# Performance work log

Measured on AMD Instinct MI355X. Metric: run time of the kernel, lower is better.

## Reference

```python
import jax, jax.numpy as jnp
import numpy as np

CUTOFF = 3.5          # angular_cutoff (init kwarg)
EPS = 1e-7            # keras.backend.epsilon()
CLIP_MIN = 1e-10      # tf.clip_by_value min on Carnot denominators
B, N = 8, 32
MLP_DIMS = [(9, 64), (64, 64), (64, 64), (64, 64), (64, 64), (64, 128), (128, 256)]


def _he(key, fan_in, fan_out):
    return jax.random.normal(key, (fan_in, fan_out), jnp.float32) * np.float32(np.sqrt(2.0 / fan_in))


def setup_inputs() -> dict:
    key = jax.random.key(0)
    k_pos, k_sp, k_w, k_b = jax.random.split(key, 4)
    # realistic symmetric distance matrix with zero diagonal, from random 3D positions
    pos = jax.random.uniform(k_pos, (B, N, 3), jnp.float32) * 9.0
    diff = pos[:, :, None, :] - pos[:, None, :, :]
    D = jnp.sqrt(jnp.sum(diff * diff, axis=-1) + 1e-12)
    D = D * (1.0 - jnp.eye(N, dtype=jnp.float32))
    species = jax.random.randint(k_sp, (B, N), 1, 10).astype(jnp.float32)
    inp = {"distance_matrices": D, "num_species_batch": species}
    for i, (fi, fo) in enumerate(MLP_DIMS):
        inp[f"W{i}"] = _he(jax.random.fold_in(k_w, i), fi, fo)
        inp[f"b{i}"] = jax.random.normal(jax.random.fold_in(k_b, i), (fo,), jnp.float32) * 0.01
    return inp


def _ang_mlp(x, W0, b0, W1, b1, W2, b2, W3, b3, W4, b4, W5, b5, W6, b6):
    # residual MLP: 9 -> 64 (x5, two residual adds) -> 128 -> 256, all tanh
    x_res = jnp.tanh(x @ W0 + b0)
    x1 = jnp.tanh(x_res @ W1 + b1)
    xb1 = x1 + x_res
    x2 = jnp.tanh(xb1 @ W2 + b2)
    x3 = jnp.tanh(x2 @ W3 + b3)
    x4 = jnp.tanh(x3 @ W4 + b4)
    xb2 = x4 + xb1
    xb3 = jnp.tanh(xb2 @ W5 + b5)
    return jnp.tanh(xb3 @ W6 + b6)


def _forward(D, S, W0, b0, W1, b1, W2, b2, W3, b3, W4, b4, W5, b5, W6, b6):
    n = D.shape[-1]
    ji, ki = jnp.triu_indices(n, k=1)                       # P = n(n-1)/2 ordered pairs j<k
    cm = (D < CUTOFF) & (D != 0.0)                          # [B,N,N]
    mask = cm[:, :, ji] & cm[:, :, ki]                      # [B,N,P] valid triplets (i;j,k)
    R_ij = D[:, :, ji]                                      # [B,N,P]
    R_ik = D[:, :, ki]
    R_jk = jnp.broadcast_to(D[:, ji, ki][:, None, :], R_ij.shape)
    z_i = jnp.broadcast_to(S[:, :, None], R_ij.shape)
    z_j = jnp.broadcast_to(S[:, ji][:, None, :], R_ij.shape)
    z_k = jnp.broadcast_to(S[:, ki][:, None, :], R_ij.shape)
    # Carnot formula for the three cosines of the triangle (i,j,k)
    clip = lambda d: jnp.maximum(d, CLIP_MIN)
    c_i = (R_ij**2 + R_ik**2 - R_jk**2) / clip(2.0 * R_ij * R_ik)
    c_j = (R_ij**2 + R_jk**2 - R_ik**2) / clip(2.0 * R_ij * R_jk)
    c_k = (R_ik**2 + R_jk**2 - R_ij**2) / clip(2.0 * R_ik * R_jk)
    geo = jnp.stack([
        R_ij + R_ik + R_jk,
        R_ij * R_ik + R_ij * R_jk + R_ik * R_jk,
        R_ij * R_ik * R_jk,
    ], axis=-1)                                             # [B,N,P,3]
    chem = jnp.stack([
        z_i + z_j + z_k,
        c_i + c_j + c_k,
        z_i * (z_j + z_k) + z_j * z_k - c_i * (c_j + c_k) - c_j * c_k,
        z_i * (c_j + c_k) + c_i * (z_j + z_k) + z_j * c_k + c_j * z_k,
        z_i * (z_j * z_k - c_j * c_k) - c_i * (z_j * c_k + c_j * z_k),
        z_i * (z_j * c_k + c_j * z_k) + c_i * (z_j * z_k - c_j * c_k),
    ], axis=-1)                                             # [B,N,P,6]
    geo = geo / (jnp.linalg.norm(geo, axis=-1, keepdims=True) + EPS)
    chem = chem / (jnp.linalg.norm(chem, axis=-1, keepdims=True) + EPS)
    feat = jnp.concatenate([geo, chem], axis=-1)            # [B,N,P,9]
    out = _ang_mlp(feat, W0, b0, W1, b1, W2, b2, W3, b3, W4, b4, W5, b5, W6, b6)  # [B,N,P,256]
    f_c = lambda d: 0.5 * jnp.cos(np.float32(np.pi) * d / CUTOFF) + 0.5
    w = jnp.where(mask, f_c(R_ij) * f_c(R_ik), 0.0)[..., None]
    GA = jnp.sum(out * w, axis=2)                           # scatter-add over triplets -> [B,N,256]
    return GA / (jnp.linalg.norm(GA, axis=-1, keepdims=True) + EPS)


def reference(distance_matrices, num_species_batch, W0, b0, W1, b1, W2, b2, W3, b3, W4, b4, W5, b5, W6, b6):
    return _forward(distance_matrices, num_species_batch, W0, b0, W1, b1, W2, b2, W3, b3, W4, b4, W5, b5, W6, b6)
```

## Files before the change

### kernel.cpp

```cpp
#include <hip/hip_runtime.h>
#include <math.h>

#define NB 8
#define NA 32
#define NCELL 256
#define NPAIR 496
#define SLOT 496
#define FST 10
#define TC 16
#define XS 20
#define NQ 8
#define CUTOFF_F 3.5f
#define EPS_F 1e-7f
#define CLIP_MIN_F 1e-10f
#define PI_F 3.14159274101257324f

#define PIPE_BAR4() do { \
    asm volatile("s_waitcnt lgkmcnt(0) vmcnt(4)" ::: "memory"); \
    __builtin_amdgcn_s_barrier(); \
    __builtin_amdgcn_sched_barrier(0); \
} while (0)
#define PIPE_BAR0() do { \
    asm volatile("s_waitcnt lgkmcnt(0) vmcnt(0)" ::: "memory"); \
    __builtin_amdgcn_s_barrier(); \
    __builtin_amdgcn_sched_barrier(0); \
} while (0)

__device__ __forceinline__ float fast_tanh(float x) {
    const float ax = fabsf(x);
    const float t = exp2f(fminf(2.8853900817779268f * ax, 30.0f));
    const float r = (t - 1.0f) * __builtin_amdgcn_rcpf(t + 1.0f);
    return __int_as_float((__float_as_int(x) & 0x80000000) | __float_as_int(r));
}

__global__ __launch_bounds__(256) void aev_feat(
    const float* __restrict__ D, const float* __restrict__ S,
    float* __restrict__ feat, int* __restrict__ count, float* __restrict__ GA)
{
    __shared__ float Dm[NA][NA];
    __shared__ float Sv[NA];
    __shared__ int s_T;
    const int tid = threadIdx.x;
    const int cell = blockIdx.x;
    const int b = cell >> 5, i = cell & 31;

    for (int idx = tid; idx < NA * NA; idx += 256)
        ((float*)Dm)[idx] = D[b * NA * NA + idx];
    if (tid < NA) Sv[tid] = S[b * NA + tid];
    if (tid == 0) s_T = 0;
    GA[cell * 256 + tid] = 0.f;
    __syncthreads();

    for (int p = tid; p < NPAIR; p += 256) {
        int rem = p, j = 0;
        while (rem >= 31 - j) { rem -= 31 - j; ++j; }
        const int k = j + 1 + rem;
        const float dij = Dm[i][j], dik = Dm[i][k];
        if (dij < CUTOFF_F && dij != 0.f && dik < CUTOFF_F && dik != 0.f) {
            const int slot = atomicAdd(&s_T, 1);
            const float Rij = dij, Rik = dik, Rjk = Dm[j][k];
            const float zi = Sv[i], zj = Sv[j], zk = Sv[k];
            const float ci = (Rij*Rij + Rik*Rik - Rjk*Rjk) / fmaxf(2.f*Rij*Rik, CLIP_MIN_F);
            const float cj = (Rij*Rij + Rjk*Rjk - Rik*Rik) / fmaxf(2.f*Rij*Rjk, CLIP_MIN_F);
            const float ck = (Rik*Rik + Rjk*Rjk - Rij*Rij) / fmaxf(2.f*Rik*Rjk, CLIP_MIN_F);
            float g0 = Rij + Rik + Rjk;
            float g1 = Rij*Rik + Rij*Rjk + Rik*Rjk;
            float g2 = Rij*Rik*Rjk;
            const float gn = sqrtf(g0*g0 + g1*g1 + g2*g2) + EPS_F;
            float h0 = zi + zj + zk;
            float h1 = ci + cj + ck;
            float h2 = zi*(zj + zk) + zj*zk - ci*(cj + ck) - cj*ck;
            float h3 = zi*(cj + ck) + ci*(zj + zk) + zj*ck + cj*zk;
            float h4 = zi*(zj*zk - cj*ck) - ci*(zj*ck + cj*zk);
            float h5 = zi*(zj*ck + cj*zk) + ci*(zj*zk - cj*ck);
            const float hn = sqrtf(h0*h0 + h1*h1 + h2*h2 + h3*h3 + h4*h4 + h5*h5) + EPS_F;
            const float fcij = 0.5f * cosf(PI_F * Rij / CUTOFF_F) + 0.5f;
            const float fcik = 0.5f * cosf(PI_F * Rik / CUTOFF_F) + 0.5f;
            float* fp = &feat[(cell * SLOT + slot) * FST];
            fp[0] = g0 / gn; fp[1] = g1 / gn; fp[2] = g2 / gn;
            fp[3] = h0 / hn; fp[4] = h1 / hn; fp[5] = h2 / hn;
            fp[6] = h3 / hn; fp[7] = h4 / hn; fp[8] = h5 / hn;
            fp[9] = fcij * fcik;
        }
    }
    __syncthreads();
    if (tid == 0) count[cell] = s_T;
}

__device__ __forceinline__ void cp_async16(const float* g, float* l) {
    __builtin_amdgcn_global_load_lds(
        (const __attribute__((address_space(1))) unsigned int*)g,
        (__attribute__((address_space(3))) unsigned int*)l, 16, 0, 0);
}

__device__ __forceinline__ void stage16k(const float* __restrict__ g,
                                         float* __restrict__ buf, int tid) {
    const int lane = tid & 63, w = tid >> 6;
#pragma unroll
    for (int r = 0; r < 4; ++r) {
        const int off = (w * 4 + r) * 256;
        cp_async16(g + off + lane * 4, buf + off);
    }
}

template<int K, bool RES>
__device__ __forceinline__ void compute64(
    const float* __restrict__ Wl, float bb,
    const float* __restrict__ X, float* __restrict__ Y,
    const float* __restrict__ R, int tid)
{
    const int fi = tid & 63;
    const int xo = (tid >> 6) * 4;
    float a0 = bb, a1 = bb, a2 = bb, a3 = bb;
#pragma unroll 4
    for (int k = 0; k < K; ++k) {
        const float4 xv = *(const float4*)&X[k * XS + xo];
        const float w = Wl[k * 64 + fi];
        a0 += xv.x * w; a1 += xv.y * w; a2 += xv.z * w; a3 += xv.w * w;
    }
    float4 y;
    y.x = fast_tanh(a0); y.y = fast_tanh(a1); y.z = fast_tanh(a2); y.w = fast_tanh(a3);
    if (RES) {
        const float4 r = *(const float4*)&R[fi * XS + xo];
        y.x += r.x; y.y += r.y; y.z += r.z; y.w += r.w;
    }
    *(float4*)&Y[fi * XS + xo] = y;
}

__device__ __forceinline__ void compute5_part(
    const float* __restrict__ Wl , const float* __restrict__ X,
    int k0, float (&a)[4][2], int tid)
{
    const int f = (tid & 31) * 4;
    const int t = (tid >> 5) * 2;
#pragma unroll 4
    for (int k = 0; k < 32; ++k) {
        const float4 wv = *(const float4*)&Wl[k * 128 + f];
        const float2 xv = *(const float2*)&X[(k0 + k) * XS + t];
        a[0][0] += wv.x * xv.x; a[0][1] += wv.x * xv.y;
        a[1][0] += wv.y * xv.x; a[1][1] += wv.y * xv.y;
        a[2][0] += wv.z * xv.x; a[2][1] += wv.z * xv.y;
        a[3][0] += wv.w * xv.x; a[3][1] += wv.w * xv.y;
    }
}

__device__ __forceinline__ void compute6_part(
    const float* __restrict__ Wl , const float* __restrict__ X,
    float (&c)[4][4], int f, int t)
{
#pragma unroll 2
    for (int k = 0; k < 16; ++k) {
        const float4 wv = *(const float4*)&Wl[k * 256 + f];
        const float4 xv = *(const float4*)&X[k * XS + t];
        c[0][0] += wv.x * xv.x; c[0][1] += wv.x * xv.y; c[0][2] += wv.x * xv.z; c[0][3] += wv.x * xv.w;
        c[1][0] += wv.y * xv.x; c[1][1] += wv.y * xv.y; c[1][2] += wv.y * xv.z; c[1][3] += wv.y * xv.w;
        c[2][0] += wv.z * xv.x; c[2][1] += wv.z * xv.y; c[2][2] += wv.z * xv.z; c[2][3] += wv.z * xv.w;
        c[3][0] += wv.w * xv.x; c[3][1] += wv.w * xv.y; c[3][2] += wv.w * xv.z; c[3][3] += wv.w * xv.w;
    }
}

__global__ __launch_bounds__(256) void aev_mlp(
    const float* __restrict__ feat, const int* __restrict__ count,
    const float* __restrict__ W0, const float* __restrict__ b0,
    const float* __restrict__ W1, const float* __restrict__ b1,
    const float* __restrict__ W2, const float* __restrict__ b2,
    const float* __restrict__ W3, const float* __restrict__ b3,
    const float* __restrict__ W4, const float* __restrict__ b4,
    const float* __restrict__ W5, const float* __restrict__ b5,
    const float* __restrict__ W6, const float* __restrict__ b6,
    float* __restrict__ GA)
{
    __shared__ __align__(16) float WB0[4096];
    __shared__ __align__(16) float WB1[4096];
    __shared__ __align__(16) float WB2[4096];
    __shared__ __align__(16) float W0s[576];
    __shared__ __align__(16) float Xs[9 * XS];
    __shared__ __align__(16) float U0[64 * XS];
    __shared__ __align__(16) float U1[64 * XS];
    __shared__ __align__(16) float U2[64 * XS];
    __shared__ float wsh[TC];

    const int tid = threadIdx.x;
    const int cell = blockIdx.x & 255;
    const int q = blockIdx.x >> 8;
    const int T = count[cell];
    const int nch = (T + TC - 1) / TC;
    if (q >= nch) return;

    const int fi64 = tid & 63;
    const float bias0 = b0[fi64];
    const float bias1 = b1[fi64];
    const float bias2 = b2[fi64];
    const float bias3 = b3[fi64];
    const float bias4 = b4[fi64];
    const int f5 = (tid & 31) * 4;
    const int t5 = (tid >> 5) * 2;
    const float4 bias5v = *(const float4*)&b5[f5];
    const int f6 = (tid >> 6) * 64 + (tid & 15) * 4;
    const int t6 = ((tid >> 4) & 3) * 4;
    const float4 bias6v = *(const float4*)&b6[f6];

    if (tid < 144) ((float4*)W0s)[tid] = ((const float4*)W0)[tid];

    float gacc = 0.f;

    for (int c = q; c < nch; c += NQ) {
        const int t0 = c * TC;

        stage16k(W1, WB0, tid);
        if (tid < TC * FST) {
            const int t = tid / FST, qf = tid % FST;
            const int slot = t0 + t;
            const float v = (slot < T) ? feat[(cell * SLOT + t0) * FST + tid] : 0.f;
            if (qf == 9) wsh[t] = v; else Xs[qf * XS + t] = v;
        }
        PIPE_BAR4();
        stage16k(W2, WB1, tid);
        compute64<9,  false>(W0s, bias0, Xs, U0, nullptr, tid);
        PIPE_BAR4();
        stage16k(W3, WB2, tid);
        compute64<64, true >(WB0, bias1, U0, U1, U0, tid);
        PIPE_BAR4();
        stage16k(W4, WB0, tid);
        compute64<64, false>(WB1, bias2, U1, U2, nullptr, tid);
        PIPE_BAR4();
        stage16k(W5, WB1, tid);
        compute64<64, false>(WB2, bias3, U2, U0, nullptr, tid);
        PIPE_BAR4();
        stage16k(W5 + 4096, WB2, tid);
        compute64<64, true >(WB0, bias4, U0, U2, U1, tid);
        PIPE_BAR4();

        float a5[4][2];
#pragma unroll
        for (int i = 0; i < 4; ++i) {
            const float bi = (i == 0) ? bias5v.x : (i == 1) ? bias5v.y
                           : (i == 2) ? bias5v.z : bias5v.w;
            a5[i][0] = bi; a5[i][1] = bi;
        }
        stage16k(W6, WB0, tid);
        compute5_part(WB1, U2, 0, a5, tid);
        PIPE_BAR4();
        stage16k(W6 + 4096, WB1, tid);
        compute5_part(WB2, U2, 32, a5, tid);
        {
            float* base = (f5 < 64) ? U0 : U1;
            const int fr = f5 & 63;
#pragma unroll
            for (int i = 0; i < 4; ++i) {
                float2 y;
                y.x = fast_tanh(a5[i][0]); y.y = fast_tanh(a5[i][1]);
                *(float2*)&base[(fr + i) * XS + t5] = y;
            }
        }
        PIPE_BAR4();

        float c6[4][4];
#pragma unroll
        for (int i = 0; i < 4; ++i) {
            const float bi = (i == 0) ? bias6v.x : (i == 1) ? bias6v.y
                           : (i == 2) ? bias6v.z : bias6v.w;
#pragma unroll
            for (int j = 0; j < 4; ++j) c6[i][j] = bi;
        }
        stage16k(W6 + 2 * 4096, WB2, tid);
        compute6_part(WB0, U0 + 0 * XS, c6, f6, t6);
        PIPE_BAR4();
        stage16k(W6 + 3 * 4096, WB0, tid);
        compute6_part(WB1, U0 + 16 * XS, c6, f6, t6);
        PIPE_BAR4();
        stage16k(W6 + 4 * 4096, WB1, tid);
        compute6_part(WB2, U0 + 32 * XS, c6, f6, t6);
        PIPE_BAR4();
        stage16k(W6 + 5 * 4096, WB2, tid);
        compute6_part(WB0, U0 + 48 * XS, c6, f6, t6);
        PIPE_BAR4();
        stage16k(W6 + 6 * 4096, WB0, tid);
        compute6_part(WB1, U1 + 0 * XS, c6, f6, t6);
        PIPE_BAR4();
        stage16k(W6 + 7 * 4096, WB1, tid);
        compute6_part(WB2, U1 + 16 * XS, c6, f6, t6);
        PIPE_BAR4();
        compute6_part(WB0, U1 + 32 * XS, c6, f6, t6);
        PIPE_BAR0();
        compute6_part(WB1, U1 + 48 * XS, c6, f6, t6);

        {
            const float4 wv4 = *(const float4*)&wsh[t6];
            float4 s;
            s.x = wv4.x * fast_tanh(c6[0][0]) + wv4.y * fast_tanh(c6[0][1])
                + wv4.z * fast_tanh(c6[0][2]) + wv4.w * fast_tanh(c6[0][3]);
            s.y = wv4.x * fast_tanh(c6[1][0]) + wv4.y * fast_tanh(c6[1][1])
                + wv4.z * fast_tanh(c6[1][2]) + wv4.w * fast_tanh(c6[1][3]);
            s.z = wv4.x * fast_tanh(c6[2][0]) + wv4.y * fast_tanh(c6[2][1])
                + wv4.z * fast_tanh(c6[2][2]) + wv4.w * fast_tanh(c6[2][3]);
            s.w = wv4.x * fast_tanh(c6[3][0]) + wv4.y * fast_tanh(c6[3][1])
                + wv4.z * fast_tanh(c6[3][2]) + wv4.w * fast_tanh(c6[3][3]);
            *(float4*)&U2[((f6 >> 2) << 4) + (t6 & 12)] = s;
        }
        __syncthreads();
        gacc += U2[(tid >> 2) * 16 + 0  + (tid & 3)]
              + U2[(tid >> 2) * 16 + 4  + (tid & 3)]
              + U2[(tid >> 2) * 16 + 8  + (tid & 3)]
              + U2[(tid >> 2) * 16 + 12 + (tid & 3)];
        __syncthreads();
    }

    atomicAdd(&GA[cell * 256 + tid], gacc);
}

__global__ __launch_bounds__(256) void aev_norm(
    const float* __restrict__ GA, float* __restrict__ out)
{
    __shared__ float wred[4];
    const int tid = threadIdx.x;
    const int cell = blockIdx.x;
    const float v = GA[cell * 256 + tid];
    float ss = v * v;
#pragma unroll
    for (int off = 32; off > 0; off >>= 1) ss += __shfl_down(ss, off);
    if ((tid & 63) == 0) wred[tid >> 6] = ss;
    __syncthreads();
    const float tot = wred[0] + wred[1] + wred[2] + wred[3];
    out[cell * 256 + tid] = v / (sqrtf(tot) + EPS_F);
}

extern "C" void kernel_launch(void* const* d_in, const int* in_sizes, int n_in,
                              void* d_out, int out_size, void* d_ws, size_t ws_size,
                              hipStream_t stream)
{
    const float* D  = (const float*)d_in[0];
    const float* S  = (const float*)d_in[1];
    const float* W0 = (const float*)d_in[2];  const float* b0 = (const float*)d_in[3];
    const float* W1 = (const float*)d_in[4];  const float* b1 = (const float*)d_in[5];
    const float* W2 = (const float*)d_in[6];  const float* b2 = (const float*)d_in[7];
    const float* W3 = (const float*)d_in[8];  const float* b3 = (const float*)d_in[9];
    const float* W4 = (const float*)d_in[10]; const float* b4 = (const float*)d_in[11];
    const float* W5 = (const float*)d_in[12]; const float* b5 = (const float*)d_in[13];
    const float* W6 = (const float*)d_in[14]; const float* b6 = (const float*)d_in[15];
    float* out = (float*)d_out;

    float* feat  = (float*)d_ws;
    int*   count = (int*)(feat + NCELL * SLOT * FST);
    float* GA    = (float*)(count + 256);

    aev_feat<<<dim3(NCELL), dim3(256), 0, stream>>>(D, S, feat, count, GA);
    aev_mlp<<<dim3(NCELL * NQ), dim3(256), 0, stream>>>(
        feat, count, W0, b0, W1, b1, W2, b2, W3, b3, W4, b4, W5, b5, W6, b6, GA);
    aev_norm<<<dim3(NCELL), dim3(256), 0, stream>>>(GA, out);
}
```

Before: 115.3 us.

## Double triplet chunk to 32 with 512-thread blocks in MLP kernel

Doubles the per-block triplet chunk from 16 to 32 and the block size from 256 to 512 threads. Each staged weight tile is then reused across twice as many triplets, and the copy work per thread is halved. Per-layer thread-to-output mappings, the final reduction layout and the input-buffer aliasing (Xs now shares U2) are reworked to fit. The costs are fewer blocks per cell (NQ 8 to 4), more padding waste on partial chunks, larger LDS activation buffers, and an extra barrier before the reduction write.

```diff
diff --git a/kernel.cpp b/kernel.cpp
--- a/kernel.cpp
+++ b/kernel.cpp
@@ -7,16 +7,16 @@
 #define NPAIR 496
 #define SLOT 496
 #define FST 10
-#define TC 16
-#define XS 20
-#define NQ 8
+#define TC 32
+#define XS 36
+#define NQ 4
 #define CUTOFF_F 3.5f
 #define EPS_F 1e-7f
 #define CLIP_MIN_F 1e-10f
 #define PI_F 3.14159274101257324f
 
-#define PIPE_BAR4() do { \
-    asm volatile("s_waitcnt lgkmcnt(0) vmcnt(4)" ::: "memory"); \
+#define PIPE_BAR2() do { \
+    asm volatile("s_waitcnt lgkmcnt(0) vmcnt(2)" ::: "memory"); \
     __builtin_amdgcn_s_barrier(); \
     __builtin_amdgcn_sched_barrier(0); \
 } while (0)
@@ -97,8 +97,8 @@
                                          float* __restrict__ buf, int tid) {
     const int lane = tid & 63, w = tid >> 6;
 #pragma unroll
-    for (int r = 0; r < 4; ++r) {
-        const int off = (w * 4 + r) * 256;
+    for (int r = 0; r < 2; ++r) {
+        const int off = (w * 2 + r) * 256;
         cp_async16(g + off + lane * 4, buf + off);
     }
 }
@@ -159,7 +159,7 @@
     }
 }
 
-__global__ __launch_bounds__(256) void aev_mlp(
+__global__ __launch_bounds__(512) void aev_mlp(
     const float* __restrict__ feat, const int* __restrict__ count,
     const float* __restrict__ W0, const float* __restrict__ b0,
     const float* __restrict__ W1, const float* __restrict__ b1,
@@ -174,11 +174,12 @@
     __shared__ __align__(16) float WB1[4096];
     __shared__ __align__(16) float WB2[4096];
     __shared__ __align__(16) float W0s[576];
-    __shared__ __align__(16) float Xs[9 * XS];
     __shared__ __align__(16) float U0[64 * XS];
     __shared__ __align__(16) float U1[64 * XS];
     __shared__ __align__(16) float U2[64 * XS];
     __shared__ float wsh[TC];
+
+    float* const Xs = U2;
 
     const int tid = threadIdx.x;
     const int cell = blockIdx.x & 255;
@@ -196,8 +197,8 @@
     const int f5 = (tid & 31) * 4;
     const int t5 = (tid >> 5) * 2;
     const float4 bias5v = *(const float4*)&b5[f5];
-    const int f6 = (tid >> 6) * 64 + (tid & 15) * 4;
-    const int t6 = ((tid >> 4) & 3) * 4;
+    const int f6 = (tid >> 7) * 64 + (tid & 15) * 4;
+    const int t6 = ((tid >> 4) & 7) * 4;
     const float4 bias6v = *(const float4*)&b6[f6];
 
     if (tid < 144) ((float4*)W0s)[tid] = ((const float4*)W0)[tid];
@@ -214,22 +215,22 @@
             const float v = (slot < T) ? feat[(cell * SLOT + t0) * FST + tid] : 0.f;
             if (qf == 9) wsh[t] = v; else Xs[qf * XS + t] = v;
         }
-        PIPE_BAR4();
+        PIPE_BAR2();
         stage16k(W2, WB1, tid);
         compute64<9,  false>(W0s, bias0, Xs, U0, nullptr, tid);
-        PIPE_BAR4();
+        PIPE_BAR2();
         stage16k(W3, WB2, tid);
         compute64<64, true >(WB0, bias1, U0, U1, U0, tid);
-        PIPE_BAR4();
+        PIPE_BAR2();
         stage16k(W4, WB0, tid);
         compute64<64, false>(WB1, bias2, U1, U2, nullptr, tid);
-        PIPE_BAR4();
+        PIPE_BAR2();
         stage16k(W5, WB1, tid);
         compute64<64, false>(WB2, bias3, U2, U0, nullptr, tid);
-        PIPE_BAR4();
+        PIPE_BAR2();
         stage16k(W5 + 4096, WB2, tid);
         compute64<64, true >(WB0, bias4, U0, U2, U1, tid);
-        PIPE_BAR4();
+        PIPE_BAR2();
 
         float a5[4][2];
 #pragma unroll
@@ -240,7 +241,7 @@
         }
         stage16k(W6, WB0, tid);
         compute5_part(WB1, U2, 0, a5, tid);
-        PIPE_BAR4();
+        PIPE_BAR2();
         stage16k(W6 + 4096, WB1, tid);
         compute5_part(WB2, U2, 32, a5, tid);
         {
@@ -253,7 +254,7 @@
                 *(float2*)&base[(fr + i) * XS + t5] = y;
             }
         }
-        PIPE_BAR4();
+        PIPE_BAR2();
 
         float c6[4][4];
 #pragma unroll
@@ -265,22 +266,22 @@
         }
         stage16k(W6 + 2 * 4096, WB2, tid);
         compute6_part(WB0, U0 + 0 * XS, c6, f6, t6);
-        PIPE_BAR4();
+        PIPE_BAR2();
         stage16k(W6 + 3 * 4096, WB0, tid);
         compute6_part(WB1, U0 + 16 * XS, c6, f6, t6);
-        PIPE_BAR4();
+        PIPE_BAR2();
         stage16k(W6 + 4 * 4096, WB1, tid);
         compute6_part(WB2, U0 + 32 * XS, c6, f6, t6);
-        PIPE_BAR4();
+        PIPE_BAR2();
         stage16k(W6 + 5 * 4096, WB2, tid);
         compute6_part(WB0, U0 + 48 * XS, c6, f6, t6);
-        PIPE_BAR4();
+        PIPE_BAR2();
         stage16k(W6 + 6 * 4096, WB0, tid);
         compute6_part(WB1, U1 + 0 * XS, c6, f6, t6);
-        PIPE_BAR4();
+        PIPE_BAR2();
         stage16k(W6 + 7 * 4096, WB1, tid);
         compute6_part(WB2, U1 + 16 * XS, c6, f6, t6);
-        PIPE_BAR4();
+        PIPE_BAR2();
         compute6_part(WB0, U1 + 32 * XS, c6, f6, t6);
         PIPE_BAR0();
         compute6_part(WB1, U1 + 48 * XS, c6, f6, t6);
@@ -296,17 +297,20 @@
                 + wv4.z * fast_tanh(c6[2][2]) + wv4.w * fast_tanh(c6[2][3]);
             s.w = wv4.x * fast_tanh(c6[3][0]) + wv4.y * fast_tanh(c6[3][1])
                 + wv4.z * fast_tanh(c6[3][2]) + wv4.w * fast_tanh(c6[3][3]);
-            *(float4*)&U2[((f6 >> 2) << 4) + (t6 & 12)] = s;
+            __syncthreads();
+            *(float4*)&U0[(t6 >> 2) * 256 + f6] = s;
         }
         __syncthreads();
-        gacc += U2[(tid >> 2) * 16 + 0  + (tid & 3)]
-              + U2[(tid >> 2) * 16 + 4  + (tid & 3)]
-              + U2[(tid >> 2) * 16 + 8  + (tid & 3)]
-              + U2[(tid >> 2) * 16 + 12 + (tid & 3)];
+        if (tid < 256) {
+#pragma unroll
+            for (int tg = 0; tg < 8; ++tg)
+                gacc += U0[tg * 256 + tid];
+        }
         __syncthreads();
     }
 
-    atomicAdd(&GA[cell * 256 + tid], gacc);
+    if (tid < 256)
+        atomicAdd(&GA[cell * 256 + tid], gacc);
 }
 
 __global__ __launch_bounds__(256) void aev_norm(
@@ -345,7 +349,7 @@
     float* GA    = (float*)(count + 256);
 
     aev_feat<<<dim3(NCELL), dim3(256), 0, stream>>>(D, S, feat, count, GA);
-    aev_mlp<<<dim3(NCELL * NQ), dim3(256), 0, stream>>>(
+    aev_mlp<<<dim3(NCELL * NQ), dim3(512), 0, stream>>>(
         feat, count, W0, b0, W1, b1, W2, b2, W3, b3, W4, b4, W5, b5, W6, b6, GA);
     aev_norm<<<dim3(NCELL), dim3(256), 0, stream>>>(GA, out);
 }
```

Result: slower. 132.6 us (+15.0%).

## Compact MLP work list and fuse final normalization into last-finishing block

Applied to the files above, without the earlier changes.

The feature kernel now builds a compacted list of (cell, chunk) work items with an atomic counter, so MLP blocks index into that list instead of launching a fixed grid where many blocks exit early. The separate normalization kernel is removed. The last MLP block to finish each cell, found via a per-cell done counter and threadfence, normalizes GA and writes the output. This drops one kernel launch and the empty blocks, at the cost of an extra memset, atomics and a completion-detection protocol.

```diff
diff --git a/kernel.cpp b/kernel.cpp
--- a/kernel.cpp
+++ b/kernel.cpp
@@ -10,6 +10,7 @@
 #define TC 16
 #define XS 20
 #define NQ 8
+#define MAXW (NCELL * NQ)
 #define CUTOFF_F 3.5f
 #define EPS_F 1e-7f
 #define CLIP_MIN_F 1e-10f
@@ -35,7 +36,9 @@
 
 __global__ __launch_bounds__(256) void aev_feat(
     const float* __restrict__ D, const float* __restrict__ S,
-    float* __restrict__ feat, int* __restrict__ count, float* __restrict__ GA)
+    float* __restrict__ feat, int* __restrict__ count, int* __restrict__ nblocks,
+    int* __restrict__ donecnt, int* __restrict__ wlist, int* __restrict__ total,
+    float* __restrict__ GA)
 {
     __shared__ float Dm[NA][NA];
     __shared__ float Sv[NA];
@@ -47,7 +50,7 @@
     for (int idx = tid; idx < NA * NA; idx += 256)
         ((float*)Dm)[idx] = D[b * NA * NA + idx];
     if (tid < NA) Sv[tid] = S[b * NA + tid];
-    if (tid == 0) s_T = 0;
+    if (tid == 0) { s_T = 0; donecnt[cell] = 0; }
     GA[cell * 256 + tid] = 0.f;
     __syncthreads();
 
@@ -84,7 +87,16 @@
         }
     }
     __syncthreads();
-    if (tid == 0) count[cell] = s_T;
+    if (tid == 0) {
+        const int T = s_T;
+        count[cell] = T;
+        const int nch = (T + TC - 1) / TC;
+        const int nb = max(1, min(nch, NQ));
+        nblocks[cell] = nb;
+        const int base = atomicAdd(total, nb);
+        for (int w = 0; w < nb; ++w)
+            wlist[base + w] = (cell << 4) | w;
+    }
 }
 
 __device__ __forceinline__ void cp_async16(const float* g, float* l) {
@@ -161,6 +173,8 @@
 
 __global__ __launch_bounds__(256) void aev_mlp(
     const float* __restrict__ feat, const int* __restrict__ count,
+    const int* __restrict__ nblocks, int* __restrict__ donecnt,
+    const int* __restrict__ wlist, const int* __restrict__ total,
     const float* __restrict__ W0, const float* __restrict__ b0,
     const float* __restrict__ W1, const float* __restrict__ b1,
     const float* __restrict__ W2, const float* __restrict__ b2,
@@ -168,7 +182,7 @@
     const float* __restrict__ W4, const float* __restrict__ b4,
     const float* __restrict__ W5, const float* __restrict__ b5,
     const float* __restrict__ W6, const float* __restrict__ b6,
-    float* __restrict__ GA)
+    float* __restrict__ GA, float* __restrict__ out)
 {
     __shared__ __align__(16) float WB0[4096];
     __shared__ __align__(16) float WB1[4096];
@@ -179,13 +193,15 @@
     __shared__ __align__(16) float U1[64 * XS];
     __shared__ __align__(16) float U2[64 * XS];
     __shared__ float wsh[TC];
+    __shared__ int s_last;
 
     const int tid = threadIdx.x;
-    const int cell = blockIdx.x & 255;
-    const int q = blockIdx.x >> 8;
+    if (blockIdx.x >= *total) return;
+    const int entry = wlist[blockIdx.x];
+    const int cell = entry >> 4;
+    const int q = entry & 15;
     const int T = count[cell];
     const int nch = (T + TC - 1) / TC;
-    if (q >= nch) return;
 
     const int fi64 = tid & 63;
     const float bias0 = b0[fi64];
@@ -307,22 +323,24 @@
     }
 
     atomicAdd(&GA[cell * 256 + tid], gacc);
-}
-
-__global__ __launch_bounds__(256) void aev_norm(
-    const float* __restrict__ GA, float* __restrict__ out)
-{
-    __shared__ float wred[4];
-    const int tid = threadIdx.x;
-    const int cell = blockIdx.x;
-    const float v = GA[cell * 256 + tid];
-    float ss = v * v;
-#pragma unroll
-    for (int off = 32; off > 0; off >>= 1) ss += __shfl_down(ss, off);
-    if ((tid & 63) == 0) wred[tid >> 6] = ss;
+    __threadfence();
+
+    if (tid == 0) {
+        const int nb = nblocks[cell];
+        s_last = (atomicAdd(&donecnt[cell], 1) == nb - 1) ? 1 : 0;
+    }
     __syncthreads();
-    const float tot = wred[0] + wred[1] + wred[2] + wred[3];
-    out[cell * 256 + tid] = v / (sqrtf(tot) + EPS_F);
+    if (s_last) {
+        __shared__ float wred[4];
+        const float v = atomicAdd(&GA[cell * 256 + tid], 0.f);
+        float ss = v * v;
+#pragma unroll
+        for (int off = 32; off > 0; off >>= 1) ss += __shfl_down(ss, off);
+        if ((tid & 63) == 0) wred[tid >> 6] = ss;
+        __syncthreads();
+        const float tot = wred[0] + wred[1] + wred[2] + wred[3];
+        out[cell * 256 + tid] = v / (sqrtf(tot) + EPS_F);
+    }
 }
 
 extern "C" void kernel_launch(void* const* d_in, const int* in_sizes, int n_in,
@@ -340,12 +358,18 @@
     const float* W6 = (const float*)d_in[14]; const float* b6 = (const float*)d_in[15];
     float* out = (float*)d_out;
 
-    float* feat  = (float*)d_ws;
-    int*   count = (int*)(feat + NCELL * SLOT * FST);
-    float* GA    = (float*)(count + 256);
-
-    aev_feat<<<dim3(NCELL), dim3(256), 0, stream>>>(D, S, feat, count, GA);
-    aev_mlp<<<dim3(NCELL * NQ), dim3(256), 0, stream>>>(
-        feat, count, W0, b0, W1, b1, W2, b2, W3, b3, W4, b4, W5, b5, W6, b6, GA);
-    aev_norm<<<dim3(NCELL), dim3(256), 0, stream>>>(GA, out);
-}
+    float* feat    = (float*)d_ws;
+    int*   count   = (int*)(feat + NCELL * SLOT * FST);
+    int*   nblocks = count + NCELL;
+    int*   donecnt = nblocks + NCELL;
+    int*   wlist   = donecnt + NCELL;
+    int*   total   = wlist + MAXW;
+    float* GA      = (float*)(total + 1);
+
+    hipMemsetAsync(total, 0, sizeof(int), stream);
+    aev_feat<<<dim3(NCELL), dim3(256), 0, stream>>>(
+        D, S, feat, count, nblocks, donecnt, wlist, total, GA);
+    aev_mlp<<<dim3(MAXW), dim3(256), 0, stream>>>(
+        feat, count, nblocks, donecnt, wlist, total,
+        W0, b0, W1, b1, W2, b2, W3, b3, W4, b4, W5, b5, W6, b6, GA, out);
+}
```

After: 134.0 us. +16.2%, slower.
